# Performance work log

Measured on AMD Instinct MI355X. Metric: run time of the kernel, lower is better.

## Reference

```python
import jax, jax.numpy as jnp
import numpy as np

N, D, E = 50000, 128, 800000


def setup_inputs() -> dict:
    key = jax.random.key(0)
    ks = jax.random.split(key, 12)
    x0 = jax.random.normal(ks[0], (N, D), dtype=jnp.float32)
    x1 = jax.random.normal(ks[1], (N, D), dtype=jnp.float32)
    edge_index = jax.random.randint(ks[2], (2, E), 0, N, dtype=jnp.int64)
    s = 0.05
    W1 = jax.random.normal(ks[3], (D, D), dtype=jnp.float32) * s
    b1 = jax.random.normal(ks[4], (D,), dtype=jnp.float32) * s
    W2 = jax.random.normal(ks[5], (D, D), dtype=jnp.float32) * s
    b2 = jax.random.normal(ks[6], (D,), dtype=jnp.float32) * s
    a1_w = jax.random.normal(ks[7], (D,), dtype=jnp.float32) * s
    a1_b = jax.random.normal(ks[8], (), dtype=jnp.float32) * s
    a2_w = jax.random.normal(ks[9], (D,), dtype=jnp.float32) * s
    a2_b = jax.random.normal(ks[10], (), dtype=jnp.float32) * s
    return {"x0": x0, "x1": x1, "edge_index": edge_index,
            "W1": W1, "b1": b1, "W2": W2, "b2": b2,
            "a1_w": a1_w, "a1_b": a1_b, "a2_w": a2_w, "a2_b": a2_b}


def reference(x0, x1, edge_index, W1, b1, W2, b2, a1_w, a1_b, a2_w, a2_b):
    # LeakyReLU(0.2) applied to both projections
    lrelu = lambda v: jnp.where(v >= 0, v, 0.2 * v)
    x0_i = lrelu(x0 @ W1.T + b1)          # [N, D]
    x0_j = lrelu(x0 @ W2.T + b2)          # [N, D]
    a1 = x0_i @ a1_w + a1_b               # [N]
    a2 = x0_j @ a2_w + a2_b               # [N]
    src, dst = edge_index[0], edge_index[1]
    # sigmoid(a_1 + a_2.T) evaluated only at the sparse edge indices
    att = jax.nn.sigmoid(a1[src] + a2[dst])            # [E]
    msg = att[:, None] * x0_j[dst]                     # [E, D]
    out = jax.ops.segment_sum(msg, src, num_segments=x0.shape[0])  # sparse.mm
    return out + x0
```

## Files before the change

### kernel.cpp

```cpp
#include <hip/hip_runtime.h>
#include <hip/hip_bf16.h>

typedef unsigned int u32;
typedef unsigned short u16;

#define DIM 128
#define LWS 136
#define CHUNK 2048

typedef __bf16 bfrag __attribute__((ext_vector_type(8)));
typedef float  facc  __attribute__((ext_vector_type(4)));

__device__ __forceinline__ float2 bfpair(u32 u) {
    union { u32 i; float f; } lo, hi;
    lo.i = (u & 0xFFFFu) << 16;
    hi.i = u & 0xFFFF0000u;
    return make_float2(lo.f, hi.f);
}
__device__ __forceinline__ float bf1(u16 h) {
    union { u32 i; float f; } a; a.i = ((u32)h) << 16; return a.f;
}
__device__ __forceinline__ u16 f2bf(float f) {
    __hip_bfloat16 h = __float2bfloat16(f);
    return *reinterpret_cast<u16*>(&h);
}
__device__ __forceinline__ u32 packbf(float x, float y) {
    return (u32)f2bf(x) | ((u32)f2bf(y) << 16);
}

template<bool BF16>
__device__ __forceinline__ float ldf(const void* p, int i) {
    if constexpr (BF16) return bf1(((const u16*)p)[i]);
    else                return ((const float*)p)[i];
}

template<bool BF16>
__device__ __forceinline__ bfrag ldfrag(const void* base, int row, int elt) {
    if constexpr (BF16) {
        const uint4* p = (const uint4*)((const u16*)base + (size_t)row * DIM + elt);
        return __builtin_bit_cast(bfrag, *p);
    } else {
        const float4* p = (const float4*)((const float*)base + (size_t)row * DIM + elt);
        float4 f0 = p[0], f1 = p[1];
        uint4 u = make_uint4(packbf(f0.x, f0.y), packbf(f0.z, f0.w),
                             packbf(f1.x, f1.y), packbf(f1.z, f1.w));
        return __builtin_bit_cast(bfrag, u);
    }
}

__global__ __launch_bounds__(64) void sniff_kernel(const u32* __restrict__ x0w,
                                                   const int* __restrict__ eiw,
                                                   int* __restrict__ flags) {
    int l = threadIdx.x;
    u32 w = x0w[l];
    u32 ef = (w >> 7) & 0xFF;
    bool inr = (ef >= 99 && ef <= 141);
    unsigned long long m1 = __ballot(inr);
    bool zodd = (eiw[2 * l + 1] == 0);
    unsigned long long m2 = __ballot(zodd);
    if (l == 0) {
        flags[0] = (__popcll(m1) >= 48) ? 1 : 0;
        flags[1] = (__popcll(m2) >= 32) ? 1 : 0;
    }
}

template<bool BF16>
__global__ __launch_bounds__(256) void proj_kernel(
    const void* __restrict__ x0v,
    const void* __restrict__ W1v, const void* __restrict__ b1v,
    const void* __restrict__ W2v, const void* __restrict__ b2v,
    const void* __restrict__ a1wv, const void* __restrict__ a1bv,
    const void* __restrict__ a2wv, const void* __restrict__ a2bv,
    u16* __restrict__ xj, float* __restrict__ a1, float* __restrict__ a2,
    const int* __restrict__ flags, int n, int nchunk, int bpg)
{
    if ((flags[0] != 0) != BF16) return;
    __shared__ u16 lw[128 * LWS];

    const int t   = threadIdx.x;
    const int grp = blockIdx.x / bpg;
    const int cb  = blockIdx.x % bpg;

    const void* Wv  = grp ? W2v  : W1v;
    const void* bv  = grp ? b2v  : b1v;
    const void* awv = grp ? a2wv : a1wv;
    const void* abv = grp ? a2bv : a1bv;
    float* aout     = grp ? a2   : a1;

    for (int j = t; j < 2048; j += 256) {
        int r = j >> 4, c = j & 15;
        uint4 u;
        if constexpr (BF16) {
            u = *(const uint4*)((const u16*)Wv + (size_t)r * DIM + c * 8);
        } else {
            const float4* p = (const float4*)((const float*)Wv + (size_t)r * DIM + c * 8);
            float4 f0 = p[0], f1 = p[1];
            u = make_uint4(packbf(f0.x, f0.y), packbf(f0.z, f0.w),
                           packbf(f1.x, f1.y), packbf(f1.z, f1.w));
        }
        *(uint4*)(lw + (size_t)r * LWS + c * 8) = u;
    }
    __syncthreads();

    const int wid = t >> 6, l = t & 63;
    const int chunk = cb * 4 + wid;
    if (chunk >= nchunk) return;
    const int r0 = chunk * 32;
    const int lr = l & 15;
    const int q  = l >> 4;

    bfrag a[2][4];
    #pragma unroll
    for (int rt = 0; rt < 2; ++rt) {
        int row = min(r0 + rt * 16 + lr, n - 1);
        #pragma unroll
        for (int k = 0; k < 4; ++k)
            a[rt][k] = ldfrag<BF16>(x0v, row, k * 32 + q * 8);
    }

    facc acc[2][8];
    #pragma unroll
    for (int rt = 0; rt < 2; ++rt)
        #pragma unroll
        for (int ct = 0; ct < 8; ++ct)
            acc[rt][ct] = (facc){0.f, 0.f, 0.f, 0.f};

    #pragma unroll
    for (int ct = 0; ct < 8; ++ct) {
        bfrag bb[4];
        const u16* lrow = lw + (size_t)(ct * 16 + lr) * LWS;
        #pragma unroll
        for (int k = 0; k < 4; ++k)
            bb[k] = *(const bfrag*)(lrow + k * 32 + q * 8);
        #pragma unroll
        for (int rt = 0; rt < 2; ++rt)
            #pragma unroll
            for (int k = 0; k < 4; ++k)
                acc[rt][ct] = __builtin_amdgcn_mfma_f32_16x16x32_bf16(
                    a[rt][k], bb[k], acc[rt][ct], 0, 0, 0);
    }

    float s[2][4] = {{0.f,0.f,0.f,0.f},{0.f,0.f,0.f,0.f}};
    #pragma unroll
    for (int ct = 0; ct < 8; ++ct) {
        float bc  = ldf<BF16>(bv,  ct * 16 + lr);
        float awc = ldf<BF16>(awv, ct * 16 + lr);
        #pragma unroll
        for (int rt = 0; rt < 2; ++rt)
            #pragma unroll
            for (int reg = 0; reg < 4; ++reg) {
                float v = acc[rt][ct][reg] + bc;
                v = v >= 0.f ? v : 0.2f * v;
                int row = r0 + rt * 16 + q * 4 + reg;
                if (grp && row < n)
                    xj[(size_t)row * DIM + ct * 16 + lr] = f2bf(v);
                s[rt][reg] = fmaf(v, awc, s[rt][reg]);
            }
    }
    #pragma unroll
    for (int off = 1; off < 16; off <<= 1)
        #pragma unroll
        for (int rt = 0; rt < 2; ++rt)
            #pragma unroll
            for (int reg = 0; reg < 4; ++reg)
                s[rt][reg] += __shfl_xor(s[rt][reg], off);
    if (lr == 0) {
        float ab = ldf<BF16>(abv, 0);
        #pragma unroll
        for (int rt = 0; rt < 2; ++rt)
            #pragma unroll
            for (int reg = 0; reg < 4; ++reg) {
                int row = r0 + rt * 16 + q * 4 + reg;
                if (row < n) aout[row] = s[rt][reg] + ab;
            }
    }
}


__global__ __launch_bounds__(256) void countH_kernel(
    const int* __restrict__ ei, u32* __restrict__ keys0,
    int* __restrict__ cnt, const int* __restrict__ flags, int ne, int nblk)
{
    __shared__ int h[256];
    const int b = blockIdx.x, t = threadIdx.x;
    h[t] = 0;
    __syncthreads();
    const bool i64 = flags[1] != 0;
    const int base = b * CHUNK;
    #pragma unroll
    for (int r = 0; r < CHUNK / 256; ++r) {
        int i = base + r * 256 + t;
        if (i < ne) {
            int src = i64 ? ei[2 * i] : ei[i];
            int dst = i64 ? ei[2 * (ne + i)] : ei[ne + i];
            u32 key = ((u32)src << 16) | (u32)dst;
            keys0[i] = key;
            atomicAdd(&h[key >> 24], 1);
        }
    }
    __syncthreads();
    cnt[t * nblk + b] = h[t];
}

__global__ __launch_bounds__(256) void scan1_kernel(
    const int* __restrict__ cnt, int* __restrict__ off,
    int* __restrict__ tot, int nblk)
{
    __shared__ int v[512];
    const int d = blockIdx.x, t = threadIdx.x;
    int c0 = (t < nblk) ? cnt[d * nblk + t] : 0;
    int c1 = (t + 256 < nblk) ? cnt[d * nblk + t + 256] : 0;
    v[t] = c0; v[t + 256] = c1;
    __syncthreads();
    for (int s = 1; s < 512; s <<= 1) {
        int a0 = v[t],      b0 = (t >= s) ? v[t - s] : 0;
        int a1 = v[t + 256], b1 = (t + 256 >= s) ? v[t + 256 - s] : 0;
        __syncthreads();
        v[t] = a0 + b0; v[t + 256] = a1 + b1;
        __syncthreads();
    }
    if (t < nblk)       off[d * nblk + t]       = v[t] - c0;
    if (t + 256 < nblk) off[d * nblk + t + 256] = v[t + 256] - c1;
    if (t == 0) tot[d] = v[511];
}

__global__ __launch_bounds__(256) void scan2_kernel(
    const int* __restrict__ tot, int* __restrict__ basev)
{
    __shared__ int v[256];
    const int t = threadIdx.x;
    int c = tot[t];
    v[t] = c;
    __syncthreads();
    for (int s = 1; s < 256; s <<= 1) {
        int a = v[t], b = (t >= s) ? v[t - s] : 0;
        __syncthreads();
        v[t] = a + b;
        __syncthreads();
    }
    basev[t] = v[t] - c;
}

__global__ __launch_bounds__(256) void reorderH_kernel(
    const u32* __restrict__ kin, u32* __restrict__ kout,
    const int* __restrict__ off, const int* __restrict__ basev,
    int ne, int nblk)
{
    __shared__ int boff[256];
    __shared__ int bcnt[256];
    const int b = blockIdx.x, t = threadIdx.x;
    const int base = b * CHUNK;
    boff[t] = basev[t] + off[t * nblk + b];
    bcnt[t] = 0;
    __syncthreads();
    #pragma unroll
    for (int r = 0; r < CHUNK / 256; ++r) {
        int i = base + r * 256 + t;
        if (i < ne) {
            u32 key = kin[i];
            int d = key >> 24;
            int rk = atomicAdd(&bcnt[d], 1);
            kout[boff[d] + rk] = key;
        }
    }
}

__global__ __launch_bounds__(256) void bucket_kernel(
    const u32* __restrict__ keys1, const int* __restrict__ basev,
    const int* __restrict__ tot, const float* __restrict__ a1,
    const float* __restrict__ a2, int* __restrict__ ptr,
    uint2* __restrict__ sorted, int n)
{
    __shared__ int cnt[256];
    __shared__ int sc[256];
    __shared__ int cur[256];
    const int b = blockIdx.x, t = threadIdx.x;
    const int base = basev[b];
    const int size = tot[b];
    cnt[t] = 0;
    __syncthreads();
    for (int i = t; i < size; i += 256)
        atomicAdd(&cnt[(keys1[base + i] >> 16) & 0xFF], 1);
    __syncthreads();
    int c = cnt[t];
    sc[t] = c;
    __syncthreads();
    for (int s = 1; s < 256; s <<= 1) {
        int a = sc[t], add = (t >= s) ? sc[t - s] : 0;
        __syncthreads();
        sc[t] = a + add;
        __syncthreads();
    }
    int ex = sc[t] - c;
    cur[t] = ex;
    int sg = (b << 8) + t;
    if (sg <= n) ptr[sg] = base + ex;
    __syncthreads();
    for (int i = t; i < size; i += 256) {
        u32 key = keys1[base + i];
        int j   = (key >> 16) & 0xFF;
        int rk  = atomicAdd(&cur[j], 1);
        int src = (int)(key >> 16);
        int dst = (int)(key & 0xFFFFu);
        float av  = a1[src] + a2[dst];
        float att = 1.0f / (1.0f + __expf(-av));
        uint2 rec; rec.x = (u32)dst; rec.y = __float_as_uint(att);
        sorted[base + rk] = rec;
    }
}

template<bool BF16>
__global__ __launch_bounds__(256) void gather_kernel(
    const int* __restrict__ ptr, const uint2* __restrict__ sorted,
    const u32* __restrict__ xjw, const void* __restrict__ x0v,
    void* __restrict__ outv, const int* __restrict__ flags, int n)
{
    if ((flags[0] != 0) != BF16) return;
    int s = blockIdx.x * 4 + (threadIdx.x >> 6);
    int l = threadIdx.x & 63;
    if (s >= n) return;

    float2 acc0, acc1;
    if constexpr (BF16) acc0 = bfpair(((const u32*)x0v)[(size_t)s * 64 + l]);
    else                acc0 = ((const float2*)x0v)[(size_t)s * 64 + l];
    acc1 = make_float2(0.f, 0.f);

    int k = ptr[s], end = ptr[s + 1];

    while (k + 8 <= end) {
        uint2 r[8];
        #pragma unroll
        for (int j = 0; j < 8; ++j) r[j] = sorted[k + j];
        u32 w[8];
        #pragma unroll
        for (int j = 0; j < 8; ++j) w[j] = xjw[(size_t)r[j].x * 64 + l];
        #pragma unroll
        for (int j = 0; j < 8; ++j) {
            float att = __uint_as_float(r[j].y);
            float2 xv = bfpair(w[j]);
            if (j & 1) { acc1.x = fmaf(att, xv.x, acc1.x);
                         acc1.y = fmaf(att, xv.y, acc1.y); }
            else       { acc0.x = fmaf(att, xv.x, acc0.x);
                         acc0.y = fmaf(att, xv.y, acc0.y); }
        }
        k += 8;
    }
    if (k + 4 <= end) {
        uint2 r[4];
        #pragma unroll
        for (int j = 0; j < 4; ++j) r[j] = sorted[k + j];
        u32 w[4];
        #pragma unroll
        for (int j = 0; j < 4; ++j) w[j] = xjw[(size_t)r[j].x * 64 + l];
        #pragma unroll
        for (int j = 0; j < 4; ++j) {
            float att = __uint_as_float(r[j].y);
            float2 xv = bfpair(w[j]);
            if (j & 1) { acc1.x = fmaf(att, xv.x, acc1.x);
                         acc1.y = fmaf(att, xv.y, acc1.y); }
            else       { acc0.x = fmaf(att, xv.x, acc0.x);
                         acc0.y = fmaf(att, xv.y, acc0.y); }
        }
        k += 4;
    }
    for (; k < end; ++k) {
        uint2 cur = sorted[k];
        float att = __uint_as_float(cur.y);
        float2 xv = bfpair(xjw[(size_t)cur.x * 64 + l]);
        acc0.x = fmaf(att, xv.x, acc0.x);
        acc0.y = fmaf(att, xv.y, acc0.y);
    }
    acc0.x += acc1.x;
    acc0.y += acc1.y;

    if constexpr (BF16) ((u32*)outv)[(size_t)s * 64 + l] = packbf(acc0.x, acc0.y);
    else                ((float2*)outv)[(size_t)s * 64 + l] = acc0;
}

extern "C" void kernel_launch(void* const* d_in, const int* in_sizes, int n_in,
                              void* d_out, int out_size, void* d_ws, size_t ws_size,
                              hipStream_t stream)
{
    const void* x0  = d_in[0];
    const int*  ei  = (const int*)d_in[2];
    const void* W1  = d_in[3];
    const void* b1  = d_in[4];
    const void* W2  = d_in[5];
    const void* b2  = d_in[6];
    const void* a1w = d_in[7];
    const void* a1b = d_in[8];
    const void* a2w = d_in[9];
    const void* a2b = d_in[10];

    const int n = in_sizes[0] / DIM;
    const int e = in_sizes[2] / 2;
    const int nblk = (e + CHUNK - 1) / CHUNK;

    char* ws = (char*)d_ws;
    int* flags = (int*)ws;
    size_t off = 1024;
    u16* xj = (u16*)(ws + off);
    off += (size_t)n * DIM * sizeof(u16);   off = (off + 255) & ~(size_t)255;
    float* a1 = (float*)(ws + off);
    off += (size_t)n * sizeof(float);       off = (off + 255) & ~(size_t)255;
    float* a2 = (float*)(ws + off);
    off += (size_t)n * sizeof(float);       off = (off + 255) & ~(size_t)255;
    u32* keys0 = (u32*)(ws + off);
    off += (size_t)e * sizeof(u32);         off = (off + 255) & ~(size_t)255;
    u32* keys1 = (u32*)(ws + off);
    off += (size_t)e * sizeof(u32);         off = (off + 255) & ~(size_t)255;
    int* cntH = (int*)(ws + off);
    off += (size_t)256 * nblk * sizeof(int); off = (off + 255) & ~(size_t)255;
    int* offH = (int*)(ws + off);
    off += (size_t)256 * nblk * sizeof(int); off = (off + 255) & ~(size_t)255;
    int* totH = (int*)(ws + off);  off += 1024;
    int* baseH = (int*)(ws + off); off += 1024;
    int* ptr = (int*)(ws + off);
    off += (size_t)(n + 1) * sizeof(int);   off = (off + 255) & ~(size_t)255;
    uint2* sorted = (uint2*)(ws + off);

    sniff_kernel<<<1, 64, 0, stream>>>((const u32*)x0, ei, flags);

    const int nchunk = (n + 31) / 32;
    const int bpg = (nchunk + 3) / 4;
    proj_kernel<true ><<<2 * bpg, 256, 0, stream>>>(x0, W1, b1, W2, b2, a1w, a1b,
                                                    a2w, a2b, xj, a1, a2, flags, n, nchunk, bpg);
    proj_kernel<false><<<2 * bpg, 256, 0, stream>>>(x0, W1, b1, W2, b2, a1w, a1b,
                                                    a2w, a2b, xj, a1, a2, flags, n, nchunk, bpg);

    countH_kernel<<<nblk, 256, 0, stream>>>(ei, keys0, cntH, flags, e, nblk);
    scan1_kernel<<<256, 256, 0, stream>>>(cntH, offH, totH, nblk);
    scan2_kernel<<<1, 256, 0, stream>>>(totH, baseH);
    reorderH_kernel<<<nblk, 256, 0, stream>>>(keys0, keys1, offH, baseH, e, nblk);
    const int nbucket = (n >> 8) + 1;
    bucket_kernel<<<nbucket, 256, 0, stream>>>(keys1, baseH, totH, a1, a2,
                                               ptr, sorted, n);

    int gblocks = (n + 3) / 4;
    gather_kernel<true ><<<gblocks, 256, 0, stream>>>(ptr, sorted, (const u32*)xj,
                                                      x0, d_out, flags, n);
    gather_kernel<false><<<gblocks, 256, 0, stream>>>(ptr, sorted, (const u32*)xj,
                                                      x0, d_out, flags, n);
}
```

Baseline: 203.2 us.

## Fuse projection with edge counting, pack attention to 16 bits, widen gather unroll

Merges the projection and histogram-count kernels into one launch, interleaving projection blocks and count blocks so the two stages can run concurrently. The dtype check moves to runtime so one gather launch replaces two. Each sorted edge record shrinks from 8 to 4 bytes by quantizing attention to 16-bit fixed point packed next to the destination index, which halves that traffic. The gather main loop unroll grows from 8 to 16. Quantizing attention to 1/65535 steps adds error, and the larger unroll raises register pressure.

```diff
diff --git a/kernel.cpp b/kernel.cpp
--- a/kernel.cpp
+++ b/kernel.cpp
@@ -65,21 +65,18 @@
 }
 
 template<bool BF16>
-__global__ __launch_bounds__(256) void proj_kernel(
+__device__ __forceinline__ void proj_body(
+    u16* lw, int pid, int t,
     const void* __restrict__ x0v,
     const void* __restrict__ W1v, const void* __restrict__ b1v,
     const void* __restrict__ W2v, const void* __restrict__ b2v,
     const void* __restrict__ a1wv, const void* __restrict__ a1bv,
     const void* __restrict__ a2wv, const void* __restrict__ a2bv,
     u16* __restrict__ xj, float* __restrict__ a1, float* __restrict__ a2,
-    const int* __restrict__ flags, int n, int nchunk, int bpg)
-{
-    if ((flags[0] != 0) != BF16) return;
-    __shared__ u16 lw[128 * LWS];
-
-    const int t   = threadIdx.x;
-    const int grp = blockIdx.x / bpg;
-    const int cb  = blockIdx.x % bpg;
+    int n, int nchunk, int bpg)
+{
+    const int grp = pid / bpg;
+    const int cb  = pid % bpg;
 
     const void* Wv  = grp ? W2v  : W1v;
     const void* bv  = grp ? b2v  : b1v;
@@ -176,30 +173,53 @@
     }
 }
 
-
-__global__ __launch_bounds__(256) void countH_kernel(
-    const int* __restrict__ ei, u32* __restrict__ keys0,
-    int* __restrict__ cnt, const int* __restrict__ flags, int ne, int nblk)
-{
+__global__ __launch_bounds__(256) void proj_count_kernel(
+    const void* __restrict__ x0v,
+    const void* __restrict__ W1v, const void* __restrict__ b1v,
+    const void* __restrict__ W2v, const void* __restrict__ b2v,
+    const void* __restrict__ a1wv, const void* __restrict__ a1bv,
+    const void* __restrict__ a2wv, const void* __restrict__ a2bv,
+    u16* __restrict__ xj, float* __restrict__ a1, float* __restrict__ a2,
+    const int* __restrict__ ei, u32* __restrict__ keys0, int* __restrict__ cnt,
+    const int* __restrict__ flags, int n, int ne, int nchunk, int bpg,
+    int nblk, int S)
+{
+    __shared__ u16 lw[128 * LWS];
     __shared__ int h[256];
     const int b = blockIdx.x, t = threadIdx.x;
-    h[t] = 0;
-    __syncthreads();
-    const bool i64 = flags[1] != 0;
-    const int base = b * CHUNK;
-    #pragma unroll
-    for (int r = 0; r < CHUNK / 256; ++r) {
-        int i = base + r * 256 + t;
-        if (i < ne) {
-            int src = i64 ? ei[2 * i] : ei[i];
-            int dst = i64 ? ei[2 * (ne + i)] : ei[ne + i];
-            u32 key = ((u32)src << 16) | (u32)dst;
-            keys0[i] = key;
-            atomicAdd(&h[key >> 24], 1);
-        }
-    }
-    __syncthreads();
-    cnt[t * nblk + b] = h[t];
+    const int nbp = 2 * bpg;
+
+    if (b % S != 0) {
+        int hb = (b / S) * (S - 1) + (b % S) - 1;
+        if (hb >= nblk) return;
+        h[t] = 0;
+        __syncthreads();
+        const bool i64 = flags[1] != 0;
+        const int base = hb * CHUNK;
+        #pragma unroll
+        for (int r = 0; r < CHUNK / 256; ++r) {
+            int i = base + r * 256 + t;
+            if (i < ne) {
+                int src = i64 ? ei[2 * i] : ei[i];
+                int dst = i64 ? ei[2 * (ne + i)] : ei[ne + i];
+                u32 key = ((u32)src << 16) | (u32)dst;
+                keys0[i] = key;
+                atomicAdd(&h[key >> 24], 1);
+            }
+        }
+        __syncthreads();
+        cnt[t * nblk + hb] = h[t];
+        return;
+    }
+
+    const int pid = b / S;
+    if (pid >= nbp) return;
+    if (flags[0] != 0)
+        proj_body<true >(lw, pid, t, x0v, W1v, b1v, W2v, b2v, a1wv, a1bv,
+                         a2wv, a2bv, xj, a1, a2, n, nchunk, bpg);
+    else
+        proj_body<false>(lw, pid, t, x0v, W1v, b1v, W2v, b2v, a1wv, a1bv,
+                         a2wv, a2bv, xj, a1, a2, n, nchunk, bpg);
 }
 
 __global__ __launch_bounds__(256) void scan1_kernel(
@@ -269,7 +289,7 @@
     const u32* __restrict__ keys1, const int* __restrict__ basev,
     const int* __restrict__ tot, const float* __restrict__ a1,
     const float* __restrict__ a2, int* __restrict__ ptr,
-    uint2* __restrict__ sorted, int n)
+    u32* __restrict__ sorted, int n)
 {
     __shared__ int cnt[256];
     __shared__ int sc[256];
@@ -304,77 +324,96 @@
         int dst = (int)(key & 0xFFFFu);
         float av  = a1[src] + a2[dst];
         float att = 1.0f / (1.0f + __expf(-av));
-        uint2 rec; rec.x = (u32)dst; rec.y = __float_as_uint(att);
-        sorted[base + rk] = rec;
-    }
-}
-
-template<bool BF16>
+        u32 a16 = (u32)lrintf(att * 65535.0f);
+        sorted[base + rk] = (a16 << 16) | (u32)dst;
+    }
+}
+
+#define ATTDEC(r) ((float)((r) >> 16) * (1.0f / 65535.0f))
+
 __global__ __launch_bounds__(256) void gather_kernel(
-    const int* __restrict__ ptr, const uint2* __restrict__ sorted,
+    const int* __restrict__ ptr, const u32* __restrict__ sorted,
     const u32* __restrict__ xjw, const void* __restrict__ x0v,
     void* __restrict__ outv, const int* __restrict__ flags, int n)
 {
-    if ((flags[0] != 0) != BF16) return;
+    const bool bf16 = flags[0] != 0;
     int s = blockIdx.x * 4 + (threadIdx.x >> 6);
     int l = threadIdx.x & 63;
     if (s >= n) return;
 
     float2 acc0, acc1;
-    if constexpr (BF16) acc0 = bfpair(((const u32*)x0v)[(size_t)s * 64 + l]);
-    else                acc0 = ((const float2*)x0v)[(size_t)s * 64 + l];
+    if (bf16) acc0 = bfpair(((const u32*)x0v)[(size_t)s * 64 + l]);
+    else      acc0 = ((const float2*)x0v)[(size_t)s * 64 + l];
     acc1 = make_float2(0.f, 0.f);
 
     int k = ptr[s], end = ptr[s + 1];
 
-    while (k + 8 <= end) {
-        uint2 r[8];
-        #pragma unroll
-        for (int j = 0; j < 8; ++j) r[j] = sorted[k + j];
-        u32 w[8];
-        #pragma unroll
-        for (int j = 0; j < 8; ++j) w[j] = xjw[(size_t)r[j].x * 64 + l];
-        #pragma unroll
-        for (int j = 0; j < 8; ++j) {
-            float att = __uint_as_float(r[j].y);
+    while (k + 16 <= end) {
+        u32 r[16];
+        #pragma unroll
+        for (int j = 0; j < 16; ++j) r[j] = sorted[k + j];
+        u32 w[16];
+        #pragma unroll
+        for (int j = 0; j < 16; ++j) w[j] = xjw[(size_t)(r[j] & 0xFFFFu) * 64 + l];
+        #pragma unroll
+        for (int j = 0; j < 16; ++j) {
+            float att = ATTDEC(r[j]);
             float2 xv = bfpair(w[j]);
             if (j & 1) { acc1.x = fmaf(att, xv.x, acc1.x);
                          acc1.y = fmaf(att, xv.y, acc1.y); }
             else       { acc0.x = fmaf(att, xv.x, acc0.x);
                          acc0.y = fmaf(att, xv.y, acc0.y); }
         }
-        k += 8;
-    }
-    if (k + 4 <= end) {
-        uint2 r[4];
-        #pragma unroll
-        for (int j = 0; j < 4; ++j) r[j] = sorted[k + j];
-        u32 w[4];
-        #pragma unroll
-        for (int j = 0; j < 4; ++j) w[j] = xjw[(size_t)r[j].x * 64 + l];
-        #pragma unroll
-        for (int j = 0; j < 4; ++j) {
-            float att = __uint_as_float(r[j].y);
+        k += 16;
+    }
+    if (k + 8 <= end) {
+        u32 r[8];
+        #pragma unroll
+        for (int j = 0; j < 8; ++j) r[j] = sorted[k + j];
+        u32 w[8];
+        #pragma unroll
+        for (int j = 0; j < 8; ++j) w[j] = xjw[(size_t)(r[j] & 0xFFFFu) * 64 + l];
+        #pragma unroll
+        for (int j = 0; j < 8; ++j) {
+            float att = ATTDEC(r[j]);
             float2 xv = bfpair(w[j]);
             if (j & 1) { acc1.x = fmaf(att, xv.x, acc1.x);
                          acc1.y = fmaf(att, xv.y, acc1.y); }
             else       { acc0.x = fmaf(att, xv.x, acc0.x);
                          acc0.y = fmaf(att, xv.y, acc0.y); }
         }
+        k += 8;
+    }
+    if (k + 4 <= end) {
+        u32 r[4];
+        #pragma unroll
+        for (int j = 0; j < 4; ++j) r[j] = sorted[k + j];
+        u32 w[4];
+        #pragma unroll
+        for (int j = 0; j < 4; ++j) w[j] = xjw[(size_t)(r[j] & 0xFFFFu) * 64 + l];
+        #pragma unroll
+        for (int j = 0; j < 4; ++j) {
+            float att = ATTDEC(r[j]);
+            float2 xv = bfpair(w[j]);
+            if (j & 1) { acc1.x = fmaf(att, xv.x, acc1.x);
+                         acc1.y = fmaf(att, xv.y, acc1.y); }
+            else       { acc0.x = fmaf(att, xv.x, acc0.x);
+                         acc0.y = fmaf(att, xv.y, acc0.y); }
+        }
         k += 4;
     }
     for (; k < end; ++k) {
-        uint2 cur = sorted[k];
-        float att = __uint_as_float(cur.y);
-        float2 xv = bfpair(xjw[(size_t)cur.x * 64 + l]);
+        u32 cur = sorted[k];
+        float att = ATTDEC(cur);
+        float2 xv = bfpair(xjw[(size_t)(cur & 0xFFFFu) * 64 + l]);
         acc0.x = fmaf(att, xv.x, acc0.x);
         acc0.y = fmaf(att, xv.y, acc0.y);
     }
     acc0.x += acc1.x;
     acc0.y += acc1.y;
 
-    if constexpr (BF16) ((u32*)outv)[(size_t)s * 64 + l] = packbf(acc0.x, acc0.y);
-    else                ((float2*)outv)[(size_t)s * 64 + l] = acc0;
+    if (bf16) ((u32*)outv)[(size_t)s * 64 + l] = packbf(acc0.x, acc0.y);
+    else      ((float2*)outv)[(size_t)s * 64 + l] = acc0;
 }
 
 extern "C" void kernel_launch(void* const* d_in, const int* in_sizes, int n_in,
@@ -417,18 +456,19 @@
     int* baseH = (int*)(ws + off); off += 1024;
     int* ptr = (int*)(ws + off);
     off += (size_t)(n + 1) * sizeof(int);   off = (off + 255) & ~(size_t)255;
-    uint2* sorted = (uint2*)(ws + off);
+    u32* sorted = (u32*)(ws + off);
 
     sniff_kernel<<<1, 64, 0, stream>>>((const u32*)x0, ei, flags);
 
     const int nchunk = (n + 31) / 32;
     const int bpg = (nchunk + 3) / 4;
-    proj_kernel<true ><<<2 * bpg, 256, 0, stream>>>(x0, W1, b1, W2, b2, a1w, a1b,
-                                                    a2w, a2b, xj, a1, a2, flags, n, nchunk, bpg);
-    proj_kernel<false><<<2 * bpg, 256, 0, stream>>>(x0, W1, b1, W2, b2, a1w, a1b,
-                                                    a2w, a2b, xj, a1, a2, flags, n, nchunk, bpg);
-
-    countH_kernel<<<nblk, 256, 0, stream>>>(ei, keys0, cntH, flags, e, nblk);
+    const int nbp = 2 * bpg;
+    const int S = 1 + (nblk + nbp - 1) / nbp;
+    const int fgrid = nbp * S;
+
+    proj_count_kernel<<<fgrid, 256, 0, stream>>>(x0, W1, b1, W2, b2, a1w, a1b,
+        a2w, a2b, xj, a1, a2, ei, keys0, cntH, flags, n, e, nchunk, bpg, nblk, S);
+
     scan1_kernel<<<256, 256, 0, stream>>>(cntH, offH, totH, nblk);
     scan2_kernel<<<1, 256, 0, stream>>>(totH, baseH);
     reorderH_kernel<<<nblk, 256, 0, stream>>>(keys0, keys1, offH, baseH, e, nblk);
@@ -437,8 +477,6 @@
                                                ptr, sorted, n);
 
     int gblocks = (n + 3) / 4;
-    gather_kernel<true ><<<gblocks, 256, 0, stream>>>(ptr, sorted, (const u32*)xj,
-                                                      x0, d_out, flags, n);
-    gather_kernel<false><<<gblocks, 256, 0, stream>>>(ptr, sorted, (const u32*)xj,
-                                                      x0, d_out, flags, n);
-}
+    gather_kernel<<<gblocks, 256, 0, stream>>>(ptr, sorted, (const u32*)xj,
+                                               x0, d_out, flags, n);
+}
```

Measured after the change: 201.5 us. About the same (-0.8%).
